# Kernel tuning notes

Hardware: AMD Instinct MI355X
Metric: run time of the kernel (lower is better)

## Reference

```python
import jax, jax.numpy as jnp
import numpy as np

N, C, H, E = 100000, 128, 8, 600000
HD = C // H
EPS = 1e-5


def _layernorm(x, g, b):
    mu = jnp.mean(x, axis=-1, keepdims=True)
    var = jnp.var(x, axis=-1, keepdims=True)
    return (x - mu) * jax.lax.rsqrt(var + EPS) * g + b


def setup_inputs() -> dict:
    key = jax.random.key(0)
    ks = jax.random.split(key, 12)
    s = 1.0 / np.sqrt(C)
    x = jax.random.normal(ks[0], (N, C), dtype=jnp.float32)
    edge_index = jax.random.randint(ks[1], (2, E), 0, N, dtype=jnp.int64)
    # linear weights stored [in, out]
    Wq = jax.random.normal(ks[2], (C, C), jnp.float32) * s
    Wk = jax.random.normal(ks[3], (C, C), jnp.float32) * s
    Wv = jax.random.normal(ks[4], (C, C), jnp.float32) * s
    Wo = jax.random.normal(ks[5], (C, C), jnp.float32) * s
    W1 = jax.random.normal(ks[6], (C, 4 * C), jnp.float32) * s
    W2 = jax.random.normal(ks[7], (4 * C, C), jnp.float32) * (1.0 / np.sqrt(4 * C))
    return {
        'x': x, 'edge_index': edge_index,
        'Wq': Wq, 'bq': jnp.zeros((C,), jnp.float32),
        'Wk': Wk, 'bk': jnp.zeros((C,), jnp.float32),
        'Wv': Wv, 'bv': jnp.zeros((C,), jnp.float32),
        'Wo': Wo, 'bo': jnp.zeros((C,), jnp.float32),
        'W1': W1, 'b1': jnp.zeros((4 * C,), jnp.float32),
        'W2': W2, 'b2': jnp.zeros((C,), jnp.float32),
        'g1': jnp.ones((C,), jnp.float32), 'beta1': jnp.zeros((C,), jnp.float32),
        'g2': jnp.ones((C,), jnp.float32), 'beta2': jnp.zeros((C,), jnp.float32),
    }


def reference(x, edge_index, Wq, bq, Wk, bk, Wv, bv, Wo, bo,
              W1, b1, W2, b2, g1, beta1, g2, beta2):
    src = edge_index[0]  # x_j (source nodes)
    dst = edge_index[1]  # x_i (target nodes, aggregation index)

    residual = x
    h = _layernorm(x, g1, beta1)

    # project at node level, then gather per edge (same math as per-edge proj)
    Q = h @ Wq + bq  # [N, C]
    K = h @ Wk + bk
    V = h @ Wv + bv

    q = Q[dst].reshape(E, H, HD)
    k = K[src].reshape(E, H, HD)
    v = V[src].reshape(E, H, HD)

    attn = jnp.sum(q * k, axis=-1) / np.sqrt(HD)  # [E, H]
    attn = jax.nn.softmax(attn, axis=-1)          # softmax over heads (per source)
    msg = (v * attn[..., None]).reshape(E, C)     # [E, C]

    aggr = jax.ops.segment_sum(msg, dst, num_segments=N)  # [N, C]
    out = aggr @ Wo + bo
    x = out + residual

    residual = x
    h = _layernorm(x, g2, beta2)
    h = jax.nn.relu(h @ W1 + b1) @ W2 + b2
    return h + residual
```

## Files before the change

kernel.cpp:

```cpp
#include <hip/hip_runtime.h>
#include <hip/hip_bf16.h>

#define C_DIM 128
#define EPS_LN 1e-5f

typedef short bf16x8 __attribute__((ext_vector_type(8)));
typedef float f32x4  __attribute__((ext_vector_type(4)));
typedef __hip_bfloat16 bf16;

__device__ inline unsigned short f2bu(float f) {
    bf16 h = __float2bfloat16(f);
    return *reinterpret_cast<unsigned short*>(&h);
}
__device__ inline float blo(unsigned int u) { return __uint_as_float(u << 16); }
__device__ inline float bhi(unsigned int u) { return __uint_as_float(u & 0xffff0000u); }
__device__ inline ushort4 pack4(float a, float b, float c, float d) {
    ushort4 r; r.x = f2bu(a); r.y = f2bu(b); r.z = f2bu(c); r.w = f2bu(d); return r;
}

__global__ __launch_bounds__(256) void wconv_all(
    const float* __restrict__ Wq, const float* __restrict__ Wk,
    const float* __restrict__ Wv, const float* __restrict__ Wo,
    const float* __restrict__ W1, const float* __restrict__ W2,
    const float* __restrict__ bq, const float* __restrict__ bk,
    const float* __restrict__ bv, bf16* __restrict__ dst) {
    int idx = blockIdx.x * 256 + threadIdx.x;
    if (idx < 65536) {
        int r = idx >> 14, o = idx & 16383;
        int k = o >> 7, nn = o & 127;
        const float* W = (r == 0) ? Wq : (r == 1) ? Wk : (r == 2) ? Wv : Wo;
        dst[(r << 14) + nn * 128 + k] = __float2bfloat16(W[o]);
    } else if (idx < 131072) {
        int o = idx - 65536;
        int k = o >> 9, nn = o & 511;
        dst[65536 + nn * 128 + k] = __float2bfloat16(W1[o]);
    } else if (idx < 196608) {
        int o = idx - 131072;
        int k = o >> 7, nn = o & 127;
        dst[131072 + nn * 512 + k] = __float2bfloat16(W2[o]);
    } else if (idx < 196992) {
        int j = idx - 196608;
        int grp = j >> 7, col = j & 127;
        const float* bp = (grp == 0) ? bq : (grp == 1) ? bk : bv;
        ((float*)(dst + 196608))[j] = bp[col];
    }
}

__global__ __launch_bounds__(256) void zeroi_kernel(int* __restrict__ p, int n) {
    int i = blockIdx.x * 256 + threadIdx.x;
    if (i < n) p[i] = 0;
}

__global__ __launch_bounds__(256) void ln_kernel(
    const float* __restrict__ x, const float* __restrict__ g,
    const float* __restrict__ b, bf16* __restrict__ out, int n) {
    int wave = threadIdx.x >> 6;
    int lane = threadIdx.x & 63;
    int row = blockIdx.x * 4 + wave;
    if (row >= n) return;
    float2 v = ((const float2*)(x + (size_t)row * C_DIM))[lane];
    float s  = v.x + v.y;
    float ss = v.x * v.x + v.y * v.y;
    #pragma unroll
    for (int o = 1; o < 64; o <<= 1) {
        s  += __shfl_xor(s, o);
        ss += __shfl_xor(ss, o);
    }
    float mu  = s * (1.0f / C_DIM);
    float var = ss * (1.0f / C_DIM) - mu * mu;
    float rs  = rsqrtf(var + EPS_LN);
    float2 gg = ((const float2*)g)[lane];
    float2 bb = ((const float2*)b)[lane];
    __hip_bfloat162 o2;
    o2.x = __float2bfloat16((v.x - mu) * rs * gg.x + bb.x);
    o2.y = __float2bfloat16((v.y - mu) * rs * gg.y + bb.y);
    ((__hip_bfloat162*)(out + (size_t)row * C_DIM))[lane] = o2;
}

template<bool OUTBF16, bool RELU, bool FUSE_LN, int KSTEPS>
__global__ __launch_bounds__(256) void gemm_lds(
    const bf16* __restrict__ A, int lda,
    const bf16* __restrict__ Bt, int Kfull,
    const float* __restrict__ biasBase,
    void* __restrict__ Cd, int ldc, size_t obStride,
    const float* __restrict__ resid, int ldres,
    int M,
    const float* __restrict__ g, const float* __restrict__ be,
    bf16* __restrict__ h2) {
    __shared__ bf16 As[128][136];
    __shared__ bf16 Bs[128][136];
    int tid  = threadIdx.x;
    int lane = tid & 63;
    int w    = tid >> 6;
    int m = lane & 15, q = lane >> 4;
    int row0 = blockIdx.x * 128;
    const bf16* Bbase = Bt + (size_t)blockIdx.y * 128 * Kfull;

    f32x4 acc[2][8];
    #pragma unroll
    for (int rt = 0; rt < 2; rt++)
        #pragma unroll
        for (int ct = 0; ct < 8; ct++) acc[rt][ct] = (f32x4){0.f, 0.f, 0.f, 0.f};

    int sr = tid >> 1, sch = tid & 1;
    int gr = row0 + sr;

    for (int kt = 0; kt < KSTEPS; kt++) {
        {
            const uint4* gp = (const uint4*)(A + (size_t)gr * lda + kt * 128 + sch * 64);
            uint4* sp = (uint4*)&As[sr][sch * 64];
            if (gr < M) {
                #pragma unroll
                for (int i = 0; i < 8; i++) sp[i] = gp[i];
            } else {
                uint4 z = make_uint4(0, 0, 0, 0);
                #pragma unroll
                for (int i = 0; i < 8; i++) sp[i] = z;
            }
        }
        {
            const uint4* gp = (const uint4*)(Bbase + (size_t)sr * Kfull + kt * 128 + sch * 64);
            uint4* sp = (uint4*)&Bs[sr][sch * 64];
            #pragma unroll
            for (int i = 0; i < 8; i++) sp[i] = gp[i];
        }
        __syncthreads();
        #pragma unroll
        for (int ks = 0; ks < 4; ks++) {
            bf16x8 af0 = *(const bf16x8*)&As[w * 32 + m][ks * 32 + q * 8];
            bf16x8 af1 = *(const bf16x8*)&As[w * 32 + 16 + m][ks * 32 + q * 8];
            #pragma unroll
            for (int ct = 0; ct < 8; ct++) {
                bf16x8 bf = *(const bf16x8*)&Bs[ct * 16 + m][ks * 32 + q * 8];
                acc[0][ct] = __builtin_amdgcn_mfma_f32_16x16x32_bf16(bf, af0, acc[0][ct], 0, 0, 0);
                acc[1][ct] = __builtin_amdgcn_mfma_f32_16x16x32_bf16(bf, af1, acc[1][ct], 0, 0, 0);
            }
        }
        if (kt + 1 < KSTEPS) __syncthreads();
    }

    #pragma unroll
    for (int rt = 0; rt < 2; rt++) {
        int row = row0 + w * 32 + rt * 16 + m;
        bool valid = row < M;
        float vals[8][4];
        #pragma unroll
        for (int ct = 0; ct < 8; ct++) {
            int col = ct * 16 + q * 4;
            float4 bv = make_float4(0.f, 0.f, 0.f, 0.f);
            if (biasBase) bv = *(const float4*)(biasBase + blockIdx.y * 128 + col);
            float4 rv = make_float4(0.f, 0.f, 0.f, 0.f);
            if (resid && valid) rv = *(const float4*)(resid + (size_t)row * ldres + col);
            vals[ct][0] = acc[rt][ct][0] + bv.x + rv.x;
            vals[ct][1] = acc[rt][ct][1] + bv.y + rv.y;
            vals[ct][2] = acc[rt][ct][2] + bv.z + rv.z;
            vals[ct][3] = acc[rt][ct][3] + bv.w + rv.w;
        }
        if (FUSE_LN) {
            float s1 = 0.f, s2 = 0.f;
            #pragma unroll
            for (int ct = 0; ct < 8; ct++)
                #pragma unroll
                for (int r = 0; r < 4; r++) { s1 += vals[ct][r]; s2 += vals[ct][r] * vals[ct][r]; }
            s1 += __shfl_xor(s1, 16); s1 += __shfl_xor(s1, 32);
            s2 += __shfl_xor(s2, 16); s2 += __shfl_xor(s2, 32);
            float mu  = s1 * (1.0f / 128.f);
            float var = s2 * (1.0f / 128.f) - mu * mu;
            float rs  = rsqrtf(var + EPS_LN);
            if (valid) {
                #pragma unroll
                for (int ct = 0; ct < 8; ct++) {
                    int col = ct * 16 + q * 4;
                    *(float4*)((float*)Cd + (size_t)row * ldc + col) =
                        make_float4(vals[ct][0], vals[ct][1], vals[ct][2], vals[ct][3]);
                    float4 gg = *(const float4*)(g + col);
                    float4 bb = *(const float4*)(be + col);
                    *(ushort4*)(h2 + (size_t)row * 128 + col) =
                        pack4((vals[ct][0] - mu) * rs * gg.x + bb.x,
                              (vals[ct][1] - mu) * rs * gg.y + bb.y,
                              (vals[ct][2] - mu) * rs * gg.z + bb.z,
                              (vals[ct][3] - mu) * rs * gg.w + bb.w);
                }
            }
        } else if (valid) {
            #pragma unroll
            for (int ct = 0; ct < 8; ct++) {
                int col = ct * 16 + q * 4;
                float v0 = vals[ct][0], v1 = vals[ct][1];
                float v2 = vals[ct][2], v3 = vals[ct][3];
                if (RELU) {
                    v0 = fmaxf(v0, 0.f); v1 = fmaxf(v1, 0.f);
                    v2 = fmaxf(v2, 0.f); v3 = fmaxf(v3, 0.f);
                }
                if (OUTBF16) {
                    *(ushort4*)((bf16*)Cd + blockIdx.y * obStride + (size_t)row * ldc + col) =
                        pack4(v0, v1, v2, v3);
                } else {
                    *(float4*)((float*)Cd + blockIdx.y * obStride + (size_t)row * ldc + col) =
                        make_float4(v0, v1, v2, v3);
                }
            }
        }
    }
}

__device__ inline float dot8(uint4 a, uint4 b) {
    return blo(a.x) * blo(b.x) + bhi(a.x) * bhi(b.x)
         + blo(a.y) * blo(b.y) + bhi(a.y) * bhi(b.y)
         + blo(a.z) * blo(b.z) + bhi(a.z) * bhi(b.z)
         + blo(a.w) * blo(b.w) + bhi(a.w) * bhi(b.w);
}

__global__ __launch_bounds__(256) void attn_kernel(
    const bf16* __restrict__ Q, const bf16* __restrict__ K,
    const int* __restrict__ eidx, float* __restrict__ attn, int E_) {
    int gw = blockIdx.x * 4 + (threadIdx.x >> 6);
    int lane = threadIdx.x & 63;
    int e = gw * 8 + (lane >> 3);
    int h = lane & 7;
    bool v = e < E_;
    int src = v ? eidx[e] : 0;
    int dst = v ? eidx[E_ + e] : 0;
    const uint4* qp = (const uint4*)(Q + (size_t)dst * 128 + h * 16);
    const uint4* kp = (const uint4*)(K + (size_t)src * 128 + h * 16);
    uint4 q0 = qp[0], q1 = qp[1];
    uint4 k0 = kp[0], k1 = kp[1];
    float s = (dot8(q0, k0) + dot8(q1, k1)) * 0.25f;
    float mx = s;
    mx = fmaxf(mx, __shfl_xor(mx, 1));
    mx = fmaxf(mx, __shfl_xor(mx, 2));
    mx = fmaxf(mx, __shfl_xor(mx, 4));
    float ex = expf(s - mx);
    float sum = ex;
    sum += __shfl_xor(sum, 1);
    sum += __shfl_xor(sum, 2);
    sum += __shfl_xor(sum, 4);
    if (v) attn[(size_t)e * 8 + h] = ex / sum;
}

__global__ __launch_bounds__(256) void hist_kernel(
    const int* __restrict__ eidx, int* __restrict__ deg, int E_) {
    int e = blockIdx.x * 256 + threadIdx.x;
    if (e >= E_) return;
    atomicAdd(&deg[eidx[E_ + e]], 1);
}

__global__ __launch_bounds__(256) void alloc_kernel(
    const int* __restrict__ deg, int* __restrict__ start,
    int* __restrict__ cursor, int* __restrict__ counter, int n) {
    int i = blockIdx.x * 256 + threadIdx.x;
    if (i >= n) return;
    int d = deg[i];
    int s = atomicAdd(counter, d);
    start[i] = s;
    cursor[i] = s;
}

__global__ __launch_bounds__(256) void scatter_kernel(
    const int* __restrict__ eidx, int* __restrict__ cursor,
    int2* __restrict__ edata, int E_) {
    int e = blockIdx.x * 256 + threadIdx.x;
    if (e >= E_) return;
    int src = eidx[e];
    int dst = eidx[E_ + e];
    int pos = atomicAdd(&cursor[dst], 1);
    edata[pos] = make_int2(src, e);
}

__global__ __launch_bounds__(256) void aggr_kernel(
    const bf16* __restrict__ V, const float* __restrict__ attnW,
    const int* __restrict__ start, const int* __restrict__ deg,
    const int2* __restrict__ edata, bf16* __restrict__ ag, int n) {
    int wave = threadIdx.x >> 6;
    int lane = threadIdx.x & 63;
    int i = blockIdx.x * 4 + wave;
    if (i >= n) return;
    int s = start[i], d = deg[i];
    int h = lane >> 3;
    float ax = 0.f, ay = 0.f, bx = 0.f, by = 0.f;
    int j = s, e_ = s + d;
    for (; j + 2 <= e_; j += 2) {
        int2 e0 = edata[j], e1 = edata[j + 1];
        float a0 = attnW[(size_t)e0.y * 8 + h];
        float a1 = attnW[(size_t)e1.y * 8 + h];
        unsigned u0 = ((const unsigned*)(V + (size_t)e0.x * 128))[lane];
        unsigned u1 = ((const unsigned*)(V + (size_t)e1.x * 128))[lane];
        ax += a0 * blo(u0); ay += a0 * bhi(u0);
        bx += a1 * blo(u1); by += a1 * bhi(u1);
    }
    if (j < e_) {
        int2 e0 = edata[j];
        float a0 = attnW[(size_t)e0.y * 8 + h];
        unsigned u0 = ((const unsigned*)(V + (size_t)e0.x * 128))[lane];
        ax += a0 * blo(u0); ay += a0 * bhi(u0);
    }
    ax += bx; ay += by;
    __hip_bfloat162 o2;
    o2.x = __float2bfloat16(ax);
    o2.y = __float2bfloat16(ay);
    ((__hip_bfloat162*)(ag + (size_t)i * 128))[lane] = o2;
}

extern "C" void kernel_launch(void* const* d_in, const int* in_sizes, int n_in,
                              void* d_out, int out_size, void* d_ws, size_t ws_size,
                              hipStream_t stream) {
    const float* x   = (const float*)d_in[0];
    const int*  eidx = (const int*)d_in[1];
    const float* Wq = (const float*)d_in[2];  const float* bq = (const float*)d_in[3];
    const float* Wk = (const float*)d_in[4];  const float* bk = (const float*)d_in[5];
    const float* Wv = (const float*)d_in[6];  const float* bv = (const float*)d_in[7];
    const float* Wo = (const float*)d_in[8];  const float* bo = (const float*)d_in[9];
    const float* W1 = (const float*)d_in[10]; const float* b1 = (const float*)d_in[11];
    const float* W2 = (const float*)d_in[12]; const float* b2 = (const float*)d_in[13];
    const float* g1 = (const float*)d_in[14]; const float* be1 = (const float*)d_in[15];
    const float* g2 = (const float*)d_in[16]; const float* be2 = (const float*)d_in[17];
    float* out = (float*)d_out;

    int n  = in_sizes[0] / C_DIM;
    int E_ = in_sizes[1] / 2;
    size_t nf = (size_t)n * 128;

    bf16* Wt    = (bf16*)d_ws;
    float* bqkv = (float*)(Wt + 196608);
    bf16* reg0  = (bf16*)(bqkv + 384);
    bf16* h1 = reg0;
    bf16* Qb = reg0 + nf;
    bf16* Kb = reg0 + 2 * nf;
    bf16* Vb = reg0 + 3 * nf;
    bf16* uB = reg0;
    bf16* ag = reg0 + 4 * nf;
    char* r2 = (char*)(ag + nf);
    float* attnW = (float*)r2;
    int2* edata  = (int2*)(attnW + (size_t)E_ * 8);
    int*  ideg   = (int*)(edata + E_);
    int*  counter = ideg + n;
    int*  istart  = ideg + n + 1;
    int*  icursor = istart + n;
    bf16* h2 = (bf16*)r2;

    dim3 b256(256);
    dim3 lnGrid((n + 3) / 4);
    int rb = (n + 127) / 128;
    dim3 eGrid8((E_ + 31) / 32);
    dim3 eGrid((E_ + 255) / 256);
    dim3 nGrid((n + 255) / 256);
    dim3 n1Grid((n + 1 + 255) / 256);
    dim3 n4Grid((n + 3) / 4);

    wconv_all<<<dim3(770), b256, 0, stream>>>(Wq, Wk, Wv, Wo, W1, W2, bq, bk, bv, Wt);
    zeroi_kernel<<<n1Grid, b256, 0, stream>>>(ideg, n + 1);
    ln_kernel<<<lnGrid, b256, 0, stream>>>(x, g1, be1, h1, n);
    gemm_lds<true, false, false, 1><<<dim3(rb, 3), b256, 0, stream>>>(
        h1, 128, Wt, 128, bqkv, Qb, 128, nf, nullptr, 0, n, nullptr, nullptr, nullptr);
    attn_kernel<<<eGrid8, b256, 0, stream>>>(Qb, Kb, eidx, attnW, E_);
    hist_kernel<<<eGrid, b256, 0, stream>>>(eidx, ideg, E_);
    alloc_kernel<<<nGrid, b256, 0, stream>>>(ideg, istart, icursor, counter, n);
    scatter_kernel<<<eGrid, b256, 0, stream>>>(eidx, icursor, edata, E_);
    aggr_kernel<<<n4Grid, b256, 0, stream>>>(Vb, attnW, istart, ideg, edata, ag, n);
    gemm_lds<false, false, true, 1><<<dim3(rb, 1), b256, 0, stream>>>(
        ag, 128, Wt + 49152, 128, bo, out, 128, 0, x, 128, n, g2, be2, h2);
    gemm_lds<true, true, false, 1><<<dim3(rb, 4), b256, 0, stream>>>(
        h2, 128, Wt + 65536, 128, b1, uB, 512, 128, nullptr, 0, n, nullptr, nullptr, nullptr);
    gemm_lds<false, false, false, 4><<<dim3(rb, 1), b256, 0, stream>>>(
        uB, 512, Wt + 131072, 512, b2, out, 128, 0, out, 128, n, nullptr, nullptr, nullptr);
}
```

Measured before the change: 517.0 us.

## Fuse FFN up and down projections into one kernel keeping hidden in LDS

Replaces the two FFN GEMM launches with one kernel. Each block loads its 128 rows once, computes each 128-wide chunk of the 512-wide ReLU hidden layer with MFMA, stores that chunk as bf16 in LDS, and immediately accumulates the down projection. The 100000x512 bf16 intermediate no longer makes a round trip through global memory. In exchange, W2 fragments are read straight from global or L2 inside the inner loop without LDS staging. Each block also does serial chunk work with extra barriers and launches only one block per 128 rows, which lowers parallelism.

```diff
diff --git a/kernel.cpp b/kernel.cpp
--- a/kernel.cpp
+++ b/kernel.cpp
@@ -204,6 +204,120 @@
     }
 }
 
+__global__ __launch_bounds__(256) void ffn_fused(
+    const bf16* __restrict__ Ain,
+    const bf16* __restrict__ W1t,
+    const bf16* __restrict__ W2t,
+    const float* __restrict__ b1,
+    const float* __restrict__ b2,
+    const float* __restrict__ resid,
+    float* __restrict__ outp,
+    int M) {
+    __shared__ bf16 As[128][136];
+    __shared__ bf16 Bs[128][136];
+    int tid  = threadIdx.x;
+    int lane = tid & 63;
+    int w    = tid >> 6;
+    int m = lane & 15, q = lane >> 4;
+    int row0 = blockIdx.x * 128;
+    int sr = tid >> 1, sch = tid & 1;
+    int gr = row0 + sr;
+
+    f32x4 accO[2][8];
+    #pragma unroll
+    for (int rt = 0; rt < 2; rt++)
+        #pragma unroll
+        for (int ct = 0; ct < 8; ct++) accO[rt][ct] = (f32x4){0.f, 0.f, 0.f, 0.f};
+
+    {
+        const uint4* gp = (const uint4*)(Ain + (size_t)gr * 128 + sch * 64);
+        uint4* sp = (uint4*)&As[sr][sch * 64];
+        if (gr < M) {
+            #pragma unroll
+            for (int i = 0; i < 8; i++) sp[i] = gp[i];
+        } else {
+            uint4 z = make_uint4(0, 0, 0, 0);
+            #pragma unroll
+            for (int i = 0; i < 8; i++) sp[i] = z;
+        }
+    }
+
+    for (int c = 0; c < 4; c++) {
+        {
+            const uint4* gp = (const uint4*)(W1t + (size_t)(c * 128 + sr) * 128 + sch * 64);
+            uint4* sp = (uint4*)&Bs[sr][sch * 64];
+            #pragma unroll
+            for (int i = 0; i < 8; i++) sp[i] = gp[i];
+        }
+        __syncthreads();
+
+        f32x4 acc1[2][8];
+        #pragma unroll
+        for (int rt = 0; rt < 2; rt++)
+            #pragma unroll
+            for (int ct = 0; ct < 8; ct++) acc1[rt][ct] = (f32x4){0.f, 0.f, 0.f, 0.f};
+        #pragma unroll
+        for (int ks = 0; ks < 4; ks++) {
+            bf16x8 af0 = *(const bf16x8*)&As[w * 32 + m][ks * 32 + q * 8];
+            bf16x8 af1 = *(const bf16x8*)&As[w * 32 + 16 + m][ks * 32 + q * 8];
+            #pragma unroll
+            for (int ct = 0; ct < 8; ct++) {
+                bf16x8 bfB = *(const bf16x8*)&Bs[ct * 16 + m][ks * 32 + q * 8];
+                acc1[0][ct] = __builtin_amdgcn_mfma_f32_16x16x32_bf16(bfB, af0, acc1[0][ct], 0, 0, 0);
+                acc1[1][ct] = __builtin_amdgcn_mfma_f32_16x16x32_bf16(bfB, af1, acc1[1][ct], 0, 0, 0);
+            }
+        }
+        __syncthreads();
+
+        #pragma unroll
+        for (int rt = 0; rt < 2; rt++) {
+            int urow = w * 32 + rt * 16 + m;
+            #pragma unroll
+            for (int ct = 0; ct < 8; ct++) {
+                int col = ct * 16 + q * 4;
+                float4 bv = *(const float4*)(b1 + c * 128 + col);
+                *(ushort4*)&Bs[urow][col] = pack4(
+                    fmaxf(acc1[rt][ct][0] + bv.x, 0.f),
+                    fmaxf(acc1[rt][ct][1] + bv.y, 0.f),
+                    fmaxf(acc1[rt][ct][2] + bv.z, 0.f),
+                    fmaxf(acc1[rt][ct][3] + bv.w, 0.f));
+            }
+        }
+        __syncthreads();
+
+        #pragma unroll
+        for (int ks = 0; ks < 4; ks++) {
+            bf16x8 af0 = *(const bf16x8*)&Bs[w * 32 + m][ks * 32 + q * 8];
+            bf16x8 af1 = *(const bf16x8*)&Bs[w * 32 + 16 + m][ks * 32 + q * 8];
+            #pragma unroll
+            for (int ct = 0; ct < 8; ct++) {
+                bf16x8 bfW = *(const bf16x8*)(W2t + (size_t)(ct * 16 + m) * 512
+                                              + c * 128 + ks * 32 + q * 8);
+                accO[0][ct] = __builtin_amdgcn_mfma_f32_16x16x32_bf16(bfW, af0, accO[0][ct], 0, 0, 0);
+                accO[1][ct] = __builtin_amdgcn_mfma_f32_16x16x32_bf16(bfW, af1, accO[1][ct], 0, 0, 0);
+            }
+        }
+        if (c + 1 < 4) __syncthreads();
+    }
+
+    #pragma unroll
+    for (int rt = 0; rt < 2; rt++) {
+        int row = row0 + w * 32 + rt * 16 + m;
+        if (row >= M) continue;
+        #pragma unroll
+        for (int ct = 0; ct < 8; ct++) {
+            int col = ct * 16 + q * 4;
+            float4 bv = *(const float4*)(b2 + col);
+            float4 rv = *(const float4*)(resid + (size_t)row * 128 + col);
+            *(float4*)(outp + (size_t)row * 128 + col) = make_float4(
+                accO[rt][ct][0] + bv.x + rv.x,
+                accO[rt][ct][1] + bv.y + rv.y,
+                accO[rt][ct][2] + bv.z + rv.z,
+                accO[rt][ct][3] + bv.w + rv.w);
+        }
+    }
+}
+
 __device__ inline float dot8(uint4 a, uint4 b) {
     return blo(a.x) * blo(b.x) + bhi(a.x) * bhi(b.x)
          + blo(a.y) * blo(b.y) + bhi(a.y) * bhi(b.y)
@@ -327,7 +441,6 @@
     bf16* Qb = reg0 + nf;
     bf16* Kb = reg0 + 2 * nf;
     bf16* Vb = reg0 + 3 * nf;
-    bf16* uB = reg0;
     bf16* ag = reg0 + 4 * nf;
     char* r2 = (char*)(ag + nf);
     float* attnW = (float*)r2;
@@ -359,8 +472,6 @@
     aggr_kernel<<<n4Grid, b256, 0, stream>>>(Vb, attnW, istart, ideg, edata, ag, n);
     gemm_lds<false, false, true, 1><<<dim3(rb, 1), b256, 0, stream>>>(
         ag, 128, Wt + 49152, 128, bo, out, 128, 0, x, 128, n, g2, be2, h2);
-    gemm_lds<true, true, false, 1><<<dim3(rb, 4), b256, 0, stream>>>(
-        h2, 128, Wt + 65536, 128, b1, uB, 512, 128, nullptr, 0, n, nullptr, nullptr, nullptr);
-    gemm_lds<false, false, false, 4><<<dim3(rb, 1), b256, 0, stream>>>(
-        uB, 512, Wt + 131072, 512, b2, out, 128, 0, out, 128, n, nullptr, nullptr, nullptr);
-}
+    ffn_fused<<<dim3(rb), b256, 0, stream>>>(
+        h2, Wt + 65536, Wt + 131072, b1, b2, out, out, n);
+}
```

New measurement: 590.0 us. +14.1%, slower.

## Load GEMM tiles with direct global-to-LDS async copies and XOR swizzle

Applied to the files above, without the earlier changes.

Replaces the register-staged global-to-shared tile loads in the LDS GEMM with global_load_lds 16-byte direct copies. The padded shared arrays become unpadded, and bank conflicts are avoided with an XOR swizzle on the column slot. Out-of-range A rows are clamped to the last valid row instead of zero-filled. The aim is to cut VGPR traffic and instruction count during tile loading. The risk is that the async copies may not be properly waited on before the barrier, and the clamped rows load duplicate data.

```diff
diff --git a/kernel.cpp b/kernel.cpp
--- a/kernel.cpp
+++ b/kernel.cpp
@@ -16,6 +16,13 @@
 __device__ inline float bhi(unsigned int u) { return __uint_as_float(u & 0xffff0000u); }
 __device__ inline ushort4 pack4(float a, float b, float c, float d) {
     ushort4 r; r.x = f2bu(a); r.y = f2bu(b); r.z = f2bu(c); r.w = f2bu(d); return r;
+}
+
+__device__ inline void async_copy16(const bf16* g, bf16* s) {
+    __builtin_amdgcn_global_load_lds(
+        (const __attribute__((address_space(1))) unsigned int*)g,
+        (__attribute__((address_space(3))) unsigned int*)s,
+        16, 0, 0);
 }
 
 __global__ __launch_bounds__(256) void wconv_all(
@@ -87,8 +94,8 @@
     int M,
     const float* __restrict__ g, const float* __restrict__ be,
     bf16* __restrict__ h2) {
-    __shared__ bf16 As[128][136];
-    __shared__ bf16 Bs[128][136];
+    __shared__ bf16 As[128][128];
+    __shared__ bf16 Bs[128][128];
     int tid  = threadIdx.x;
     int lane = tid & 63;
     int w    = tid >> 6;
@@ -102,36 +109,28 @@
         #pragma unroll
         for (int ct = 0; ct < 8; ct++) acc[rt][ct] = (f32x4){0.f, 0.f, 0.f, 0.f};
 
-    int sr = tid >> 1, sch = tid & 1;
-    int gr = row0 + sr;
+    int rsub  = lane >> 4;
+    int cslot = lane & 15;
 
     for (int kt = 0; kt < KSTEPS; kt++) {
-        {
-            const uint4* gp = (const uint4*)(A + (size_t)gr * lda + kt * 128 + sch * 64);
-            uint4* sp = (uint4*)&As[sr][sch * 64];
-            if (gr < M) {
-                #pragma unroll
-                for (int i = 0; i < 8; i++) sp[i] = gp[i];
-            } else {
-                uint4 z = make_uint4(0, 0, 0, 0);
-                #pragma unroll
-                for (int i = 0; i < 8; i++) sp[i] = z;
-            }
-        }
-        {
-            const uint4* gp = (const uint4*)(Bbase + (size_t)sr * Kfull + kt * 128 + sch * 64);
-            uint4* sp = (uint4*)&Bs[sr][sch * 64];
-            #pragma unroll
-            for (int i = 0; i < 8; i++) sp[i] = gp[i];
+        #pragma unroll
+        for (int i = 0; i < 8; i++) {
+            int arow = w * 32 + i * 4 + rsub;
+            int scol = (cslot ^ (arow & 7)) << 3;
+            int garow = row0 + arow;
+            if (garow > M - 1) garow = M - 1;
+            async_copy16(A + (size_t)garow * lda + kt * 128 + scol, &As[w * 32 + i * 4][0]);
+            async_copy16(Bbase + (size_t)arow * Kfull + kt * 128 + scol, &Bs[w * 32 + i * 4][0]);
         }
         __syncthreads();
         #pragma unroll
         for (int ks = 0; ks < 4; ks++) {
-            bf16x8 af0 = *(const bf16x8*)&As[w * 32 + m][ks * 32 + q * 8];
-            bf16x8 af1 = *(const bf16x8*)&As[w * 32 + 16 + m][ks * 32 + q * 8];
+            int sofs = ((ks * 4 + q) ^ (m & 7)) << 3;
+            bf16x8 af0 = *(const bf16x8*)&As[w * 32 + m][sofs];
+            bf16x8 af1 = *(const bf16x8*)&As[w * 32 + 16 + m][sofs];
             #pragma unroll
             for (int ct = 0; ct < 8; ct++) {
-                bf16x8 bf = *(const bf16x8*)&Bs[ct * 16 + m][ks * 32 + q * 8];
+                bf16x8 bf = *(const bf16x8*)&Bs[ct * 16 + m][sofs];
                 acc[0][ct] = __builtin_amdgcn_mfma_f32_16x16x32_bf16(bf, af0, acc[0][ct], 0, 0, 0);
                 acc[1][ct] = __builtin_amdgcn_mfma_f32_16x16x32_bf16(bf, af1, acc[1][ct], 0, 0, 0);
             }
```

Result: faster. 481.4 us (-6.9%).
